# Optimization experiments

Hardware: AMD Instinct MI355X
Metric: run time of the kernel (lower is better)

Reference implementation:

```python
import jax, jax.numpy as jnp
import numpy as np

G = 8  # order of C8 rotation group

def expand_circulant(w):
    # w: [out_fields, in_fields, G] free params of a C8 regular->regular 1x1 conv.
    # Full weight: W[of*G+go, if*G+gi] = w[of, if, (go-gi) mod G]
    g = jnp.arange(G)
    idx = (g[:, None] - g[None, :]) % G            # [go, gi]
    Wf = w[:, :, idx]                              # [of, if, go, gi]
    Wf = jnp.transpose(Wf, (0, 2, 1, 3))           # [of, go, if, gi]
    return Wf.reshape(w.shape[0] * G, w.shape[1] * G)

def eq_proj(x2, w, b):
    # x2: [B, in_fields*G]; equivariant 1x1 conv = GEMM with circulant-expanded weight
    Wf = expand_circulant(w)                       # [out_fields*G, in_fields*G]
    bf = jnp.repeat(b, G)                          # per-field bias, shared across group dim
    return x2 @ Wf.T + bf

def setup_inputs() -> dict:
    key = jax.random.key(0)
    ks = jax.random.split(key, 12)
    B, d_model, n_head, d_k, d_v = 8192, 128, 8, 64, 64
    C = d_model * G                                # 1024
    s_in = 0.02
    inp = {
        'q': jax.random.normal(ks[0], (B, C, 1, 1), jnp.float32),
        'k': jax.random.normal(ks[1], (B, C, 1, 1), jnp.float32),
        'v': jax.random.normal(ks[2], (B, C, 1, 1), jnp.float32),
        'w_q': jax.random.normal(ks[3], (n_head * d_k, d_model, G), jnp.float32) * s_in,
        'b_q': jnp.zeros((n_head * d_k,), jnp.float32),
        'w_k': jax.random.normal(ks[4], (n_head * d_k, d_model, G), jnp.float32) * s_in,
        'b_k': jnp.zeros((n_head * d_k,), jnp.float32),
        'w_v': jax.random.normal(ks[5], (n_head * d_v, d_model, G), jnp.float32) * s_in,
        'b_v': jnp.zeros((n_head * d_v,), jnp.float32),
        'w_fc': jax.random.normal(ks[6], (d_model, n_head * d_v, G), jnp.float32) * s_in,
        'b_fc': jnp.zeros((d_model,), jnp.float32),
    }
    return inp

def reference(q, k, v, w_q, b_q, w_k, b_k, w_v, b_v, w_fc, b_fc):
    B, C = q.shape[0], q.shape[1]
    n_head, d_k = 8, 64
    d_v = 64
    temp = jnp.asarray(d_k ** 0.5, q.dtype)
    residual = q                                   # [B, C, 1, 1]
    q2 = q.reshape(B, C)
    k2 = k.reshape(B, C)
    v2 = v.reshape(B, C)
    # equivariant 1x1 conv projections -> [B, n_head*d_k*G]
    qp = eq_proj(q2, w_q, b_q).reshape(B, G, n_head, d_k).transpose(0, 2, 1, 3)  # [B,H,G,dk]
    kp = eq_proj(k2, w_k, b_k).reshape(B, G, n_head, d_k).transpose(0, 2, 1, 3)
    vp = eq_proj(v2, w_v, b_v).reshape(B, G, n_head, d_v).transpose(0, 2, 1, 3)
    # scaled dot-product attention over the G=8 group/orientation positions
    attn = jax.nn.softmax(jnp.einsum('bhqd,bhkd->bhqk', qp / temp, kp), axis=-1)  # [B,H,G,G]
    out = jnp.einsum('bhqk,bhkd->bhqd', attn, vp)  # [B,H,G,dv]
    # transpose(1,2) then flatten, exactly as torch .view(sz_b, -1, 1, 1)
    out = out.transpose(0, 2, 1, 3).reshape(B, G * n_head * d_v)
    out = eq_proj(out, w_fc, b_fc)                 # [B, d_model*G]
    out = out.reshape(B, C, 1, 1) + residual
    return out, attn
```

## Files before the change

### kernel.cpp

```cpp
#include <hip/hip_runtime.h>
#include <hip/hip_bf16.h>

typedef unsigned short u16;
typedef unsigned int u32;
typedef __bf16 bf16x8_t __attribute__((ext_vector_type(8)));
typedef float f32x4_t __attribute__((ext_vector_type(4)));

__device__ __forceinline__ float b2f(u16 v) {
  return __uint_as_float(((u32)v) << 16);
}
__device__ __forceinline__ u16 f2b(float f) {
  __hip_bfloat16 h = __float2bfloat16(f);
  return *reinterpret_cast<u16*>(&h);
}
__device__ __forceinline__ float blo(u32 u) { return __uint_as_float(u << 16); }
__device__ __forceinline__ float bhi(u32 u) { return __uint_as_float(u & 0xffff0000u); }

__device__ __forceinline__ void async_lds16(const u16* g, u16* l) {
  __builtin_amdgcn_global_load_lds(
      (__attribute__((address_space(1))) void*)g,
      (__attribute__((address_space(3))) void*)l, 16, 0, 0);
}

__device__ __forceinline__ void expand8(const float* __restrict__ w,
                                        u16* __restrict__ dst, int I,
                                        int kshift, int gid) {
  const int n = gid >> kshift;
  const int kc = (gid & ((1 << kshift) - 1)) * 8;
  const int K = 8 << kshift;
  const float* wp = w + (size_t)((n >> 3) * I + (kc >> 3)) * 8;
  float4 w0 = *(const float4*)wp;
  float4 w1 = *(const float4*)(wp + 4);
  float w8[8] = {w0.x, w0.y, w0.z, w0.w, w1.x, w1.y, w1.z, w1.w};
  u16 t[8];
  const int r = (n - kc) & 7;
#pragma unroll
  for (int j = 0; j < 8; ++j) t[j] = f2b(w8[(r - j) & 7]);
  *(uint4*)(dst + (size_t)n * K + kc) = *(const uint4*)t;
}

__device__ __forceinline__ void cvt8(const float* __restrict__ src,
                                     u16* __restrict__ dst, int gid) {
  const float* p = src + (size_t)gid * 8;
  float4 a = *(const float4*)p;
  float4 b = *(const float4*)(p + 4);
  u16 t[8] = {f2b(a.x), f2b(a.y), f2b(a.z), f2b(a.w),
              f2b(b.x), f2b(b.y), f2b(b.z), f2b(b.w)};
  *(uint4*)(dst + (size_t)gid * 8) = *(const uint4*)t;
}

__global__ __launch_bounds__(256) void expand_all(
    const float* __restrict__ w_q, const float* __restrict__ w_k,
    const float* __restrict__ w_v, const float* __restrict__ w_fc,
    const float* __restrict__ q, const float* __restrict__ k,
    const float* __restrict__ v, u16* __restrict__ Wq, u16* __restrict__ Wk,
    u16* __restrict__ Wv, u16* __restrict__ Wfc, u16* __restrict__ qb,
    u16* __restrict__ kb, u16* __restrict__ vb, int cblocks) {
  const int e = blockIdx.x;
  if (e < 8192) {
    const int plane = e >> 11;
    const int gid = (e & 2047) * 256 + threadIdx.x;
    if (plane == 0) expand8(w_q, Wq, 128, 7, gid);
    else if (plane == 1) expand8(w_k, Wk, 128, 7, gid);
    else if (plane == 2) expand8(w_v, Wv, 128, 7, gid);
    else expand8(w_fc, Wfc, 512, 9, gid);
  } else {
    const int ce = e - 8192;
    const int plane = ce / cblocks;
    const int gid = (ce - plane * cblocks) * 256 + threadIdx.x;
    if (plane == 0) cvt8(q, qb, gid);
    else if (plane == 1) cvt8(k, kb, gid);
    else cvt8(v, vb, gid);
  }
}

template <int TM, int TN, bool HAS_RES, bool OUT_F32>
__device__ __forceinline__ void gemm_pipe(
    const u16* __restrict__ X, const u16* __restrict__ W,
    const float* __restrict__ bias, const float* __restrict__ res,
    void* __restrict__ Yv, int M, int N, int K, int bid) {
  constexpr int LDS_A = TM * 32;
  constexpr int BUF = (TM + TN) * 32;
  constexpr int APASS = TM / 128, BPASS = TN / 128;
  constexpr int LPT = APASS + BPASS;
  constexpr int NJ = TN / 64;
  constexpr int FH = TM / 64;
  __shared__ __align__(16) u16 lds[4 * BUF];

  const int tid = threadIdx.x;
  const int grid_m = M / TM, grid_n = N / TN;
  const int nb = grid_m * grid_n;
  int pid = (bid & 7) * (nb >> 3) + (bid >> 3);
  const int nig = 8 * grid_n;
  const int group_id = pid / nig;
  const int first_m = group_id * 8;
  const int gsz = min(8, grid_m - first_m);
  const int mt = first_m + (pid % gsz);
  const int ntile = (pid % nig) / gsz;
  const int m0 = mt * TM, n0 = ntile * TN;

  const int lane = tid & 63, wave = tid >> 6;
  const int wm = (wave >> 2) * (TM / 2);
  const int wn = (wave & 3) * (TN / 4);
  const int l16 = lane & 15, quad = lane >> 4;
  const int kbl = quad ^ ((l16 >> 1) & 3);

  const int srow = tid >> 2;
  const int skbg = (tid & 3) ^ ((tid >> 3) & 3);
  const u16* pA = X + (size_t)(m0 + srow) * K + skbg * 8;
  const u16* pB = W + (size_t)(n0 + srow) * K + skbg * 8;
  const size_t rskip = (size_t)128 * K;

  const int aoff = (wm + l16) * 32 + kbl * 8;
  const int boff = LDS_A + (wn + l16) * 32 + kbl * 8;

  f32x4_t acc[2 * FH][NJ] = {};
  const int nt = K >> 5;

  auto stage = [&](int t) {
    u16* l = lds + (t & 3) * BUF;
    const u16* a = pA + t * 32;
    const u16* b = pB + t * 32;
#pragma unroll
    for (int p = 0; p < APASS; ++p)
      async_lds16(a + p * rskip, l + tid * 8 + p * 4096);
#pragma unroll
    for (int p = 0; p < BPASS; ++p)
      async_lds16(b + p * rskip, l + LDS_A + tid * 8 + p * 4096);
  };

#define WAIT_VM_LPT()                                              \
  do {                                                             \
    if constexpr (LPT == 4)                                        \
      asm volatile("s_waitcnt vmcnt(4)" ::: "memory");             \
    else if constexpr (LPT == 3)                                   \
      asm volatile("s_waitcnt vmcnt(3)" ::: "memory");             \
    else                                                           \
      asm volatile("s_waitcnt vmcnt(2)" ::: "memory");             \
  } while (0)

  bf16x8_t A0[FH], A1[FH], Bc[NJ], Bn[NJ];

  stage(0);
  __builtin_amdgcn_sched_barrier(0);
  stage(1);
  __builtin_amdgcn_sched_barrier(0);
  stage(2);
  WAIT_VM_LPT();
  __builtin_amdgcn_s_barrier();
  __builtin_amdgcn_sched_barrier(0);

  {
    const u16* la = lds + aoff;
    const u16* lb = lds + boff;
#pragma unroll
    for (int mi = 0; mi < FH; ++mi) A0[mi] = *(const bf16x8_t*)(la + mi * 512);
#pragma unroll
    for (int ni = 0; ni < NJ; ++ni) Bc[ni] = *(const bf16x8_t*)(lb + ni * 512);
  }

  auto body = [&](int t, bf16x8_t (&BCUR)[NJ], bf16x8_t (&BNXT)[NJ]) {
    if (t + 3 < nt) stage(t + 3);
    const u16* lc = lds + (t & 3) * BUF;
    const u16* ln = lds + ((t + 1) & 3) * BUF;
#pragma unroll
    for (int mi = 0; mi < FH; ++mi)
      A1[mi] = *(const bf16x8_t*)(lc + aoff + (mi + FH) * 512);
    if (t + 1 < nt) {
#pragma unroll
      for (int ni = 0; ni < NJ; ++ni)
        BNXT[ni] = *(const bf16x8_t*)(ln + boff + ni * 512);
    }
    __builtin_amdgcn_s_setprio(1);
#pragma unroll
    for (int mi = 0; mi < FH; ++mi)
#pragma unroll
      for (int ni = 0; ni < NJ; ++ni)
        acc[mi][ni] = __builtin_amdgcn_mfma_f32_16x16x32_bf16(
            A0[mi], BCUR[ni], acc[mi][ni], 0, 0, 0);
    __builtin_amdgcn_s_setprio(0);
    if (t + 1 < nt) {
#pragma unroll
      for (int mi = 0; mi < FH; ++mi)
        A0[mi] = *(const bf16x8_t*)(ln + aoff + mi * 512);
    }
    __builtin_amdgcn_s_setprio(1);
#pragma unroll
    for (int mi = 0; mi < FH; ++mi)
#pragma unroll
      for (int ni = 0; ni < NJ; ++ni)
        acc[mi + FH][ni] = __builtin_amdgcn_mfma_f32_16x16x32_bf16(
            A1[mi], BCUR[ni], acc[mi + FH][ni], 0, 0, 0);
    __builtin_amdgcn_s_setprio(0);
    if (t + 1 < nt) {
      asm volatile("s_waitcnt lgkmcnt(0)" ::: "memory");
      __builtin_amdgcn_sched_barrier(0);
      if (t + 3 < nt) WAIT_VM_LPT();
      else            asm volatile("s_waitcnt vmcnt(0)" ::: "memory");
      __builtin_amdgcn_s_barrier();
      __builtin_amdgcn_sched_barrier(0);
    }
  };

  for (int t = 0; t < nt; t += 2) {
    body(t, Bc, Bn);
    body(t + 1, Bn, Bc);
  }
#undef WAIT_VM_LPT

#pragma unroll
  for (int ni = 0; ni < NJ; ++ni) {
    const int col = n0 + wn + ni * 16 + l16;
    const float bv = bias[col >> 3];
#pragma unroll
    for (int mi = 0; mi < 2 * FH; ++mi) {
#pragma unroll
      for (int r = 0; r < 4; ++r) {
        const int rw = m0 + wm + mi * 16 + quad * 4 + r;
        float vv = acc[mi][ni][r] + bv;
        if (HAS_RES) vv += res[(size_t)rw * N + col];
        if (OUT_F32)
          ((float*)Yv)[(size_t)rw * N + col] = vv;
        else
          ((u16*)Yv)[(size_t)rw * N + col] = f2b(vv);
      }
    }
  }
}

__global__ __launch_bounds__(512, 2) void gemm_qkv256(
    const u16* __restrict__ X0, const u16* __restrict__ X1,
    const u16* __restrict__ X2, const u16* __restrict__ W0,
    const u16* __restrict__ W1, const u16* __restrict__ W2,
    const float* __restrict__ b0, const float* __restrict__ b1,
    const float* __restrict__ b2, u16* __restrict__ Y0, u16* __restrict__ Y1,
    u16* __restrict__ Y2, int M, int N, int K) {
  const int z = blockIdx.y;
  const u16* X = (z == 0) ? X0 : (z == 1) ? X1 : X2;
  const u16* W = (z == 0) ? W0 : (z == 1) ? W1 : W2;
  const float* bb = (z == 0) ? b0 : (z == 1) ? b1 : b2;
  u16* Y = (z == 0) ? Y0 : (z == 1) ? Y1 : Y2;
  gemm_pipe<256, 256, false, false>(X, W, bb, nullptr, Y, M, N, K, blockIdx.x);
}

__global__ __launch_bounds__(512, 2) void gemm_fc(
    const u16* __restrict__ X, const u16* __restrict__ W,
    const float* __restrict__ bias, const float* __restrict__ res,
    float* __restrict__ Y, int M, int N, int K) {
  gemm_pipe<128, 128, true, true>(X, W, bias, res, Y, M, N, K, blockIdx.x);
}

__global__ __launch_bounds__(256) void attn_kernel(
    const u16* __restrict__ qp, const u16* __restrict__ kp,
    const u16* __restrict__ vp, float* __restrict__ probs,
    u16* __restrict__ o, int iters) {
  __shared__ __align__(16) u16 Qs[4][8 * 72];
  __shared__ __align__(16) u16 Ks[4][8 * 72];
  __shared__ __align__(16) float Ps[4][64];
  const int tid = threadIdx.x;
  const int wave = tid >> 6;
  const int lane = tid & 63;
  const int r = lane >> 3, c = lane & 7;
  const int ls = r * 72 + c * 8;
  const int qg = r;
  const int kg = c;

  auto pairof = [&](int it) { return (it * gridDim.x + blockIdx.x) * 4 + wave; };
  auto gaddr = [&](int it) {
    const int pr = pairof(it);
    return (size_t)(pr >> 3) * 4096 + (size_t)r * 512 + (pr & 7) * 64 + c * 8;
  };

  uint4 qr = *(const uint4*)(qp + gaddr(0));
  uint4 kr = *(const uint4*)(kp + gaddr(0));

  for (int it = 0; it < iters; ++it) {
    *(uint4*)&Qs[wave][ls] = qr;
    *(uint4*)&Ks[wave][ls] = kr;
    const int pair = pairof(it);
    const int b = pair >> 3;
    const int h = pair & 7;
    float vcf[8];
#pragma unroll
    for (int k2 = 0; k2 < 8; ++k2)
      vcf[k2] = b2f(vp[(size_t)b * 4096 + (size_t)k2 * 512 + h * 64 + lane]);
    if (it + 1 < iters) {
      qr = *(const uint4*)(qp + gaddr(it + 1));
      kr = *(const uint4*)(kp + gaddr(it + 1));
    }
    float s = 0.f;
#pragma unroll
    for (int d8 = 0; d8 < 8; ++d8) {
      uint4 qa = *(const uint4*)&Qs[wave][qg * 72 + d8 * 8];
      uint4 ka = *(const uint4*)&Ks[wave][kg * 72 + d8 * 8];
      s += blo(qa.x) * blo(ka.x) + bhi(qa.x) * bhi(ka.x);
      s += blo(qa.y) * blo(ka.y) + bhi(qa.y) * bhi(ka.y);
      s += blo(qa.z) * blo(ka.z) + bhi(qa.z) * bhi(ka.z);
      s += blo(qa.w) * blo(ka.w) + bhi(qa.w) * bhi(ka.w);
    }
    s *= 0.125f;
    float mx = s;
    mx = fmaxf(mx, __shfl_xor(mx, 1));
    mx = fmaxf(mx, __shfl_xor(mx, 2));
    mx = fmaxf(mx, __shfl_xor(mx, 4));
    float e = __expf(s - mx);
    float sum = e;
    sum += __shfl_xor(sum, 1);
    sum += __shfl_xor(sum, 2);
    sum += __shfl_xor(sum, 4);
    const float p = e / sum;
    probs[(size_t)pair * 64 + lane] = p;
    Ps[wave][lane] = p;
#pragma unroll
    for (int q2 = 0; q2 < 8; ++q2) {
      float4 p0 = *(const float4*)&Ps[wave][q2 * 8];
      float4 p1 = *(const float4*)&Ps[wave][q2 * 8 + 4];
      float acc = p0.x * vcf[0] + p0.y * vcf[1] + p0.z * vcf[2] + p0.w * vcf[3] +
                  p1.x * vcf[4] + p1.y * vcf[5] + p1.z * vcf[6] + p1.w * vcf[7];
      o[(size_t)b * 4096 + q2 * 512 + h * 64 + lane] = f2b(acc);
    }
  }
}

extern "C" void kernel_launch(void* const* d_in, const int* in_sizes, int n_in,
                              void* d_out, int out_size, void* d_ws, size_t ws_size,
                              hipStream_t stream) {
  const float* q = (const float*)d_in[0];
  const float* k = (const float*)d_in[1];
  const float* v = (const float*)d_in[2];
  const float* w_q = (const float*)d_in[3];
  const float* b_q = (const float*)d_in[4];
  const float* w_k = (const float*)d_in[5];
  const float* b_k = (const float*)d_in[6];
  const float* w_v = (const float*)d_in[7];
  const float* b_v = (const float*)d_in[8];
  const float* w_fc = (const float*)d_in[9];
  const float* b_fc = (const float*)d_in[10];

  const int B = in_sizes[0] / 1024;
  float* out = (float*)d_out;
  float* probs = out + (size_t)B * 1024;

  u16* Wq = (u16*)d_ws;
  u16* Wk = Wq + (size_t)4096 * 1024;
  u16* Wv = Wk + (size_t)4096 * 1024;
  u16* Wfc = Wv + (size_t)4096 * 1024;
  u16* qb = Wfc + (size_t)4096 * 1024;
  u16* kb = qb + (size_t)B * 1024;
  u16* vb = kb + (size_t)B * 1024;
  u16* scratch = vb + (size_t)B * 1024;
  const size_t fixed_bytes =
      ((size_t)4 * 4096 * 1024 + (size_t)3 * B * 1024) * sizeof(u16);

  const size_t per_row = (size_t)(4 * 4096) * sizeof(u16);
  int chunkB = 256;
  for (int c = B; c >= 256; c >>= 1) {
    if (fixed_bytes + (size_t)c * per_row <= ws_size) { chunkB = c; break; }
  }

  u16* qp = scratch;
  u16* kp = qp + (size_t)chunkB * 4096;
  u16* vp = kp + (size_t)chunkB * 4096;
  u16* ao = vp + (size_t)chunkB * 4096;

  const int cblocks = B / 2;
  expand_all<<<8192 + 3 * cblocks, 256, 0, stream>>>(
      w_q, w_k, w_v, w_fc, q, k, v, Wq, Wk, Wv, Wfc, qb, kb, vb, cblocks);

  for (int cs = 0; cs < B; cs += chunkB) {
    const int nb_p = (chunkB / 256) * (4096 / 256);
    gemm_qkv256<<<dim3(nb_p, 3), 512, 0, stream>>>(
        qb + (size_t)cs * 1024, kb + (size_t)cs * 1024, vb + (size_t)cs * 1024,
        Wq, Wk, Wv, b_q, b_k, b_v, qp, kp, vp, chunkB, 4096, 1024);
    const int ablocks = (chunkB >= 1024) ? 2048 : chunkB * 2;
    const int aiters = (chunkB * 8) / (ablocks * 4);
    attn_kernel<<<ablocks, 256, 0, stream>>>(qp, kp, vp,
                                             probs + (size_t)cs * 512, ao, aiters);
    const int nb_fc = (chunkB / 128) * (1024 / 128);
    gemm_fc<<<nb_fc, 512, 0, stream>>>(ao, Wfc, b_fc, q + (size_t)cs * 1024,
                                       out + (size_t)cs * 1024, chunkB, 1024,
                                       4096);
  }
}
```

Before: 591.2 us.

## Replace QKV GEMM with 8-phase ping-pong pipelined 256x256 kernel using K-tile 64

Adds a dedicated QKV projection GEMM that uses 64-wide K tiles, a 128 KiB LDS double buffer split into halves, and eight phases per two K-tiles. Each phase interleaves async global-to-LDS staging of the next half-tile with MFMA on a quarter of the output tile, using s_setprio, sched barriers and explicit vmcnt/lgkmcnt waits. The goal is to overlap memory traffic with matrix math more tightly than the previous generic pipeline. The cost is many more barriers per K step and a large LDS footprint, which may limit occupancy to one block per CU despite the launch bounds.

```diff
diff --git a/kernel.cpp b/kernel.cpp
--- a/kernel.cpp
+++ b/kernel.cpp
@@ -74,6 +74,174 @@
   }
 }
 
+__global__ __launch_bounds__(512, 2) void gemm_qkv8p(
+    const u16* __restrict__ X0, const u16* __restrict__ X1,
+    const u16* __restrict__ X2, const u16* __restrict__ W0,
+    const u16* __restrict__ W1, const u16* __restrict__ W2,
+    const float* __restrict__ b0v, const float* __restrict__ b1v,
+    const float* __restrict__ b2v, u16* __restrict__ Y0, u16* __restrict__ Y1,
+    u16* __restrict__ Y2, int M, int N, int K) {
+  __shared__ __align__(16) u16 lds[65536];
+  const int z = blockIdx.y;
+  const u16* X = (z == 0) ? X0 : (z == 1) ? X1 : X2;
+  const u16* W = (z == 0) ? W0 : (z == 1) ? W1 : W2;
+  const float* bias = (z == 0) ? b0v : (z == 1) ? b1v : b2v;
+  u16* Y = (z == 0) ? Y0 : (z == 1) ? Y1 : Y2;
+
+  const int tid = threadIdx.x;
+  const int bid = blockIdx.x;
+  const int grid_m = M >> 8, grid_n = N >> 8;
+  const int nb = grid_m * grid_n;
+  int pid = (bid & 7) * (nb >> 3) + (bid >> 3);
+  const int nig = 8 * grid_n;
+  const int group_id = pid / nig;
+  const int first_m = group_id * 8;
+  const int gsz = min(8, grid_m - first_m);
+  const int mt = first_m + (pid % gsz);
+  const int ntile = (pid % nig) / gsz;
+  const int m0 = mt << 8, n0 = ntile << 8;
+
+  const int lane = tid & 63, wave = tid >> 6;
+  const int wg = wave >> 2;
+  const int wq = wave & 3;
+  const int l16 = lane & 15, quad = lane >> 4;
+  const int lswz = l16 & 7;
+
+  const u16* gA = X + (size_t)m0 * K;
+  const u16* gB = W + (size_t)n0 * K;
+  const int srow = tid >> 3;
+  const int skbg = (tid & 7) ^ (srow & 7);
+
+  f32x4_t acc[8][4] = {};
+  const int KT = K >> 6;
+  const int niter = KT >> 1;
+
+  auto stg = [&](int kt, int h, bool isB) {
+    u16* l = lds + (isB ? 32768 : 0) + ((kt & 1) * 2 + h) * 8192 + tid * 8;
+    const u16* g = (isB ? gB : gA) + (size_t)(h * 128 + srow) * K + kt * 64 +
+                   skbg * 8;
+    async_lds16(g, l);
+    async_lds16(g + (size_t)64 * K, l + 4096);
+  };
+  auto ldA = [&](int kt, int mh, bf16x8_t (&a)[8]) {
+    const u16* base = lds + ((kt & 1) * 2 + wg) * 8192 + (mh * 64 + l16) * 64;
+#pragma unroll
+    for (int mi = 0; mi < 4; ++mi)
+#pragma unroll
+      for (int ks = 0; ks < 2; ++ks)
+        a[mi * 2 + ks] = *(const bf16x8_t*)(base + mi * 1024 +
+                                            (((ks * 4 + quad) ^ lswz) * 8));
+  };
+  auto ldB = [&](int kt, int nh, bf16x8_t (&b)[4]) {
+    const u16* base = lds + 32768 + ((kt & 1) * 2 + (wq >> 1)) * 8192 +
+                      ((wq & 1) * 64 + nh * 32 + l16) * 64;
+#pragma unroll
+    for (int ni = 0; ni < 2; ++ni)
+#pragma unroll
+      for (int ks = 0; ks < 2; ++ks)
+        b[ni * 2 + ks] = *(const bf16x8_t*)(base + ni * 1024 +
+                                            (((ks * 4 + quad) ^ lswz) * 8));
+  };
+  auto mm = [&](int mh, int nh, bf16x8_t (&a)[8], bf16x8_t (&b)[4]) {
+    __builtin_amdgcn_s_setprio(1);
+#pragma unroll
+    for (int mi = 0; mi < 4; ++mi)
+#pragma unroll
+      for (int ni = 0; ni < 2; ++ni)
+#pragma unroll
+        for (int ks = 0; ks < 2; ++ks)
+          acc[mh * 4 + mi][nh * 2 + ni] = __builtin_amdgcn_mfma_f32_16x16x32_bf16(
+              a[mi * 2 + ks], b[ni * 2 + ks], acc[mh * 4 + mi][nh * 2 + ni], 0,
+              0, 0);
+    __builtin_amdgcn_s_setprio(0);
+  };
+  auto bar = [] { __builtin_amdgcn_s_barrier(); };
+  auto lgkm0 = [] {
+    asm volatile("s_waitcnt lgkmcnt(0)" ::: "memory");
+    __builtin_amdgcn_sched_barrier(0);
+  };
+  auto sched = [] { __builtin_amdgcn_sched_barrier(0); };
+
+  bf16x8_t a0[8], a1[8], b0[4], b1[4];
+
+  stg(0, 0, false); sched();
+  stg(0, 0, true);  sched();
+  stg(0, 1, false); sched();
+  stg(0, 1, true);  sched();
+  stg(1, 0, true);  sched();
+  stg(1, 0, false); sched();
+  asm volatile("s_waitcnt vmcnt(4)" ::: "memory");
+  bar();
+  sched();
+
+  for (int it = 0; it < niter; ++it) {
+    const int t = it * 2;
+    const bool more = (t + 2 < KT);
+    ldA(t, 0, a0); ldB(t, 0, b0);
+    stg(t + 1, 1, false);
+    sched(); bar(); lgkm0();
+    mm(0, 0, a0, b0);
+    bar();
+    ldB(t, 1, b1);
+    stg(t + 1, 1, true);
+    sched(); bar(); lgkm0();
+    mm(0, 1, a0, b1);
+    bar();
+    ldA(t, 1, a1);
+    if (more) stg(t + 2, 0, true);
+    sched(); bar(); lgkm0();
+    mm(1, 1, a1, b1);
+    bar();
+    if (more) stg(t + 2, 0, false);
+    sched();
+    if (more) asm volatile("s_waitcnt vmcnt(4)" ::: "memory");
+    else      asm volatile("s_waitcnt vmcnt(0)" ::: "memory");
+    bar(); lgkm0();
+    mm(1, 0, a1, b0);
+    bar();
+    ldA(t + 1, 0, a0); ldB(t + 1, 0, b0);
+    if (more) stg(t + 2, 1, false);
+    sched(); bar(); lgkm0();
+    mm(0, 0, a0, b0);
+    bar();
+    ldB(t + 1, 1, b1);
+    if (more) stg(t + 2, 1, true);
+    sched(); bar(); lgkm0();
+    mm(0, 1, a0, b1);
+    bar();
+    ldA(t + 1, 1, a1);
+    if (more) stg(t + 3, 0, true);
+    sched(); bar(); lgkm0();
+    mm(1, 1, a1, b1);
+    bar();
+    if (more) {
+      stg(t + 3, 0, false);
+      sched();
+      asm volatile("s_waitcnt vmcnt(4)" ::: "memory");
+      bar(); lgkm0();
+      mm(1, 0, a1, b0);
+      bar();
+    } else {
+      lgkm0();
+      mm(1, 0, a1, b0);
+    }
+  }
+
+#pragma unroll
+  for (int ni = 0; ni < 4; ++ni) {
+    const int col = n0 + wq * 64 + ni * 16 + l16;
+    const float bv = bias[col >> 3];
+#pragma unroll
+    for (int mi = 0; mi < 8; ++mi) {
+#pragma unroll
+      for (int r = 0; r < 4; ++r) {
+        const int rw = m0 + wg * 128 + mi * 16 + quad * 4 + r;
+        Y[(size_t)rw * N + col] = f2b(acc[mi][ni][r] + bv);
+      }
+    }
+  }
+}
+
 template <int TM, int TN, bool HAS_RES, bool OUT_F32>
 __device__ __forceinline__ void gemm_pipe(
     const u16* __restrict__ X, const u16* __restrict__ W,
@@ -226,21 +394,6 @@
       }
     }
   }
-}
-
-__global__ __launch_bounds__(512, 2) void gemm_qkv256(
-    const u16* __restrict__ X0, const u16* __restrict__ X1,
-    const u16* __restrict__ X2, const u16* __restrict__ W0,
-    const u16* __restrict__ W1, const u16* __restrict__ W2,
-    const float* __restrict__ b0, const float* __restrict__ b1,
-    const float* __restrict__ b2, u16* __restrict__ Y0, u16* __restrict__ Y1,
-    u16* __restrict__ Y2, int M, int N, int K) {
-  const int z = blockIdx.y;
-  const u16* X = (z == 0) ? X0 : (z == 1) ? X1 : X2;
-  const u16* W = (z == 0) ? W0 : (z == 1) ? W1 : W2;
-  const float* bb = (z == 0) ? b0 : (z == 1) ? b1 : b2;
-  u16* Y = (z == 0) ? Y0 : (z == 1) ? Y1 : Y2;
-  gemm_pipe<256, 256, false, false>(X, W, bb, nullptr, Y, M, N, K, blockIdx.x);
 }
 
 __global__ __launch_bounds__(512, 2) void gemm_fc(
@@ -369,7 +522,7 @@
 
   for (int cs = 0; cs < B; cs += chunkB) {
     const int nb_p = (chunkB / 256) * (4096 / 256);
-    gemm_qkv256<<<dim3(nb_p, 3), 512, 0, stream>>>(
+    gemm_qkv8p<<<dim3(nb_p, 3), 512, 0, stream>>>(
         qb + (size_t)cs * 1024, kb + (size_t)cs * 1024, vb + (size_t)cs * 1024,
         Wq, Wk, Wv, b_q, b_k, b_v, qp, kp, vp, chunkB, 4096, 1024);
     const int ablocks = (chunkB >= 1024) ? 2048 : chunkB * 2;
```

Result: faster. 578.9 us (-2.1%).
